# Performance work log

Hardware: AMD Instinct MI355X
Metric: run time of the kernel (lower is better)

The kernel has to match this reference:

```python
import jax, jax.numpy as jnp
import numpy as np

BN_EPS = 1e-5


def knn_idx(x, k):
    # x: (B, N, C) -> (B, N, k) indices of k nearest neighbors (incl. self),
    # DGCNN style: topk of negative squared distance.
    inner = jnp.einsum('bnc,bmc->bnm', x, x)
    sq = jnp.sum(x * x, axis=-1)
    neg_dist = 2.0 * inner - sq[:, :, None] - sq[:, None, :]
    _, idx = jax.lax.top_k(neg_dist, k)
    return idx


def edge_conv(x, W, b, gamma, beta, k):
    # x: (B, N, C); W: (O, 2C). One DGCNN EdgeConv block:
    # knn gather -> concat(nbr - x, x) -> conv1x1 -> BN(batch stats) -> GELU -> max over k.
    idx = knn_idx(x, k)                                   # (B, N, k)
    nbr = jax.vmap(lambda f, i: f[i])(x, idx)             # (B, N, k, C)
    ctr = jnp.broadcast_to(x[:, :, None, :], nbr.shape)
    feat = jnp.concatenate([nbr - ctr, ctr], axis=-1)     # (B, N, k, 2C)
    y = jnp.einsum('bnkc,oc->bnko', feat, W) + b          # conv 1x1
    mean = jnp.mean(y, axis=(0, 1, 2))
    var = jnp.var(y, axis=(0, 1, 2))
    y = (y - mean) * jax.lax.rsqrt(var + BN_EPS) * gamma + beta
    y = jax.nn.gelu(y, approximate=False)                 # torch nn.GELU default (erf)
    return jnp.max(y, axis=2)                             # (B, N, O)


def setup_inputs() -> dict:
    key = jax.random.key(0)
    ks = jax.random.split(key, 8)
    bs, ch, n_patches, n_samples = 4, 6, 32, 256
    dims_in = [12, 32, 64, 128, 256]
    dims_out = [16, 32, 64, 128, 256]
    inp = {'x': jax.random.normal(ks[0], (bs, ch, n_patches, n_samples), dtype=jnp.float32)}
    for i, (ci, co) in enumerate(zip(dims_in, dims_out), start=1):
        wk = jax.random.fold_in(ks[1], i)
        scale = 1.0 / np.sqrt(ci)
        inp[f'W{i}'] = (jax.random.normal(wk, (co, ci), dtype=jnp.float32) * scale)
        inp[f'b{i}'] = jnp.zeros((co,), dtype=jnp.float32)
        inp[f'g{i}'] = jnp.ones((co,), dtype=jnp.float32)
        inp[f'bt{i}'] = jnp.zeros((co,), dtype=jnp.float32)
    inp['k'] = 16
    return inp


def reference(x, W1, b1, g1, bt1, W2, b2, g2, bt2, W3, b3, g3, bt3,
              W4, b4, g4, bt4, W5, b5, g5, bt5, k):
    bs, ch, n_patches, n_samples = x.shape
    # (bs, ch, P, S) -> (bs*P, S, ch)  [channels-last point clouds]
    h = x.transpose(0, 2, 3, 1).reshape(bs * n_patches, n_samples, ch)
    h = edge_conv(h, W1, b1, g1, bt1, k)
    h = edge_conv(h, W2, b2, g2, bt2, k)
    h = edge_conv(h, W3, b3, g3, bt3, k)
    h = edge_conv(h, W4, b4, g4, bt4, k)
    h = edge_conv(h, W5, b5, g5, bt5, k)      # (bs*P, S, dim)
    dim = h.shape[-1]
    h = h.reshape(bs, n_patches, n_samples, dim)
    return h.transpose(0, 3, 1, 2)            # (bs, dim, n_patches, n_samples)
```

## Files before the change

### kernel.cpp

```cpp
#include <hip/hip_runtime.h>
#include <cmath>

#define NPTS 256
#define TOTPTS 32768
#define KNB 16

static const size_t OFF_HA   = 0;
static const size_t OFF_HB   = 4194304;
static const size_t OFF_UZ   = 6291456;
static const size_t OFF_YMAX = 23068672;
static const size_t OFF_YMIN = 31457280;
static const size_t OFF_IDX  = 39845888;
static const size_t OFF_VT   = 40370176;
static const size_t OFF_SUMS = 40458240;

__device__ __forceinline__ float gelu_erf(float v) {
  return 0.5f * v * (1.0f + erff(v * 0.70710678118654752f));
}

__global__ __launch_bounds__(256) void prep_kernel(
    const float* __restrict__ x, float* __restrict__ h0,
    const float* __restrict__ W1, const float* __restrict__ W2, const float* __restrict__ W3,
    const float* __restrict__ W4, const float* __restrict__ W5,
    float* __restrict__ Vt, double* __restrict__ sums) {
  const int stride = gridDim.x * blockDim.x;
  const int tid0 = blockIdx.x * blockDim.x + threadIdx.x;
  for (int id = tid0; id < 196608; id += stride) {
    int ch = id % 6;
    int r  = id / 6;
    int s  = r & 255;
    int p  = (r >> 8) & 31;
    int bs = r >> 13;
    h0[id] = x[(((size_t)(bs * 6 + ch) * 32 + p) << 8) + s];
  }
  for (int id = tid0; id < 87232; id += stride) {
    const float* W; int K, N2, base;
    if (id < 192)        { W = W1; K = 6;   N2 = 32;  base = 0; }
    else if (id < 1216)  { W = W2; K = 16;  N2 = 64;  base = 192; }
    else if (id < 5312)  { W = W3; K = 32;  N2 = 128; base = 1216; }
    else if (id < 21696) { W = W4; K = 64;  N2 = 256; base = 5312; }
    else                 { W = W5; K = 128; N2 = 512; base = 21696; }
    int e = id - base;
    int c = e / N2;
    int j = e - c * N2;
    int O = N2 >> 1;
    Vt[id] = (j < O) ? W[j * 2 * K + c] : W[(j - O) * 2 * K + K + c];
  }
  for (int id = tid0; id < 992; id += stride) sums[id] = 0.0;
}

template<int C>
__global__ __launch_bounds__(256) void sq_kernel(const float* __restrict__ h,
                                                 double* __restrict__ sqd) {
  const int n = blockIdx.x * 256 + threadIdx.x;
  const float* p = h + (size_t)n * C;
  double q0 = 0.0, q1 = 0.0;
  #pragma unroll
  for (int c = 0; c + 1 < C; c += 2) {
    q0 = fma((double)p[c],   (double)p[c],   q0);
    q1 = fma((double)p[c+1], (double)p[c+1], q1);
  }
  #pragma unroll
  for (int c = C & ~1; c < C; ++c) q0 = fma((double)p[c], (double)p[c], q0);
  sqd[n] = q0 + q1;
}

template<int K>
__global__ __launch_bounds__(256) void knn_fused_kernel(const float* __restrict__ h,
                                                        const double* __restrict__ sqd,
                                                        int* __restrict__ idxout) {
  constexpr int KC = (K < 16) ? K : 16;
  __shared__ unsigned long long keys[32 * 257];
  __shared__ __align__(16) float As[KC * 36];
  __shared__ __align__(16) float Bs[KC * 132];
  const int cloud = blockIdx.x >> 3;
  const int i0 = (blockIdx.x & 7) * 32;
  const float* hb = h + (size_t)cloud * NPTS * K;
  const int tid = threadIdx.x;
  const int mm = (tid & 7) * 4;
  const int jj = (tid >> 3) * 4;

  double sqi[4];
  #pragma unroll
  for (int r = 0; r < 4; ++r) sqi[r] = sqd[cloud * NPTS + i0 + mm + r];

  for (int jh = 0; jh < 2; ++jh) {
    const int j0 = jh * 128;
    double acc[4][4] = {{0.0}};
    for (int k0 = 0; k0 < K; k0 += KC) {
      for (int e = tid; e < 32 * KC; e += 256) {
        int am = e / KC, ac = e - am * KC;
        As[ac * 36 + am] = hb[(size_t)(i0 + am) * K + k0 + ac];
      }
      for (int e = tid; e < 128 * KC; e += 256) {
        int bm = e / KC, bc = e - bm * KC;
        Bs[bc * 132 + bm] = hb[(size_t)(j0 + bm) * K + k0 + bc];
      }
      __syncthreads();
      #pragma unroll
      for (int c = 0; c < KC; ++c) {
        float4 av = *(const float4*)(As + c * 36 + mm);
        float4 bv = *(const float4*)(Bs + c * 132 + jj);
        double a0 = (double)av.x, a1 = (double)av.y, a2 = (double)av.z, a3 = (double)av.w;
        double b0 = (double)bv.x, b1 = (double)bv.y, b2 = (double)bv.z, b3 = (double)bv.w;
        acc[0][0] = fma(a0, b0, acc[0][0]);
        acc[0][1] = fma(a0, b1, acc[0][1]);
        acc[0][2] = fma(a0, b2, acc[0][2]);
        acc[0][3] = fma(a0, b3, acc[0][3]);
        acc[1][0] = fma(a1, b0, acc[1][0]);
        acc[1][1] = fma(a1, b1, acc[1][1]);
        acc[1][2] = fma(a1, b2, acc[1][2]);
        acc[1][3] = fma(a1, b3, acc[1][3]);
        acc[2][0] = fma(a2, b0, acc[2][0]);
        acc[2][1] = fma(a2, b1, acc[2][1]);
        acc[2][2] = fma(a2, b2, acc[2][2]);
        acc[2][3] = fma(a2, b3, acc[2][3]);
        acc[3][0] = fma(a3, b0, acc[3][0]);
        acc[3][1] = fma(a3, b1, acc[3][1]);
        acc[3][2] = fma(a3, b2, acc[3][2]);
        acc[3][3] = fma(a3, b3, acc[3][3]);
      }
      __syncthreads();
    }
    double sqj[4];
    #pragma unroll
    for (int s = 0; s < 4; ++s) sqj[s] = sqd[cloud * NPTS + j0 + jj + s];
    #pragma unroll
    for (int r = 0; r < 4; ++r) {
      #pragma unroll
      for (int s = 0; s < 4; ++s) {
        double v = 2.0 * acc[r][s] - sqi[r] - sqj[s];
        int col = j0 + jj + s;
        keys[(mm + r) * 257 + col] =
            (((unsigned long long)__double_as_longlong(v)) & ~0xFFull) |
            (unsigned long long)col;
      }
    }
  }
  __syncthreads();

  const unsigned long long FULL = 0xFFFFFFFFFFFFFFFFull;
  const int wid  = tid >> 6;
  const int lane = tid & 63;
  const int half = lane >> 5;
  const int sub  = lane & 31;
  for (int p = 0; p < 2; ++p) {
    const int rA = p * 16 + wid * 4 + half;
    const int rC = rA + 2;
    const unsigned long long* rp1 = keys + rA * 257 + 8 * sub;
    const unsigned long long* rp2 = keys + rC * 257 + 8 * sub;
    unsigned long long a0 = rp1[0], a1 = rp1[1], a2 = rp1[2], a3 = rp1[3];
    unsigned long long a4 = rp1[4], a5 = rp1[5], a6 = rp1[6], a7 = rp1[7];
    unsigned long long b0 = rp2[0], b1 = rp2[1], b2 = rp2[2], b3 = rp2[3];
    unsigned long long b4 = rp2[4], b5 = rp2[5], b6 = rp2[6], b7 = rp2[7];

    #define CE(X, Y) { unsigned long long lo_ = (X < Y) ? X : Y; \
                       unsigned long long hi_ = (X < Y) ? Y : X; X = lo_; Y = hi_; }
    #define SORT8(v0,v1,v2,v3,v4,v5,v6,v7) \
      CE(v0,v1) CE(v2,v3) CE(v4,v5) CE(v6,v7) \
      CE(v0,v2) CE(v1,v3) CE(v4,v6) CE(v5,v7) \
      CE(v1,v2) CE(v5,v6) \
      CE(v0,v4) CE(v1,v5) CE(v2,v6) CE(v3,v7) \
      CE(v2,v4) CE(v3,v5) \
      CE(v1,v2) CE(v3,v4) CE(v5,v6)
    SORT8(a0,a1,a2,a3,a4,a5,a6,a7)
    SORT8(b0,b1,b2,b3,b4,b5,b6,b7)
    #undef SORT8
    #undef CE

    int keep1 = 0, keep2 = 0;
    for (int round = 0; round < KNB; ++round) {
      unsigned long long m1 = a0, m2 = b0, o;
      o = __shfl_xor(m1, 16); m1 = (o < m1) ? o : m1;
      o = __shfl_xor(m2, 16); m2 = (o < m2) ? o : m2;
      o = __shfl_xor(m1, 8);  m1 = (o < m1) ? o : m1;
      o = __shfl_xor(m2, 8);  m2 = (o < m2) ? o : m2;
      o = __shfl_xor(m1, 4);  m1 = (o < m1) ? o : m1;
      o = __shfl_xor(m2, 4);  m2 = (o < m2) ? o : m2;
      o = __shfl_xor(m1, 2);  m1 = (o < m1) ? o : m1;
      o = __shfl_xor(m2, 2);  m2 = (o < m2) ? o : m2;
      o = __shfl_xor(m1, 1);  m1 = (o < m1) ? o : m1;
      o = __shfl_xor(m2, 1);  m2 = (o < m2) ? o : m2;
      const int col1 = (int)(m1 & 0xFFull);
      const int col2 = (int)(m2 & 0xFFull);
      if ((col1 >> 3) == sub) {
        a0 = a1; a1 = a2; a2 = a3; a3 = a4; a4 = a5; a5 = a6; a6 = a7; a7 = FULL;
      }
      if ((col2 >> 3) == sub) {
        b0 = b1; b1 = b2; b2 = b3; b3 = b4; b4 = b5; b5 = b6; b6 = b7; b7 = FULL;
      }
      if (sub == round) { keep1 = col1; keep2 = col2; }
    }
    if (sub < KNB) {
      const int growA = cloud * NPTS + i0 + rA;
      const int growC = cloud * NPTS + i0 + rC;
      idxout[(size_t)growA * KNB + sub] = cloud * NPTS + keep1;
      idxout[(size_t)growC * KNB + sub] = cloud * NPTS + keep2;
    }
  }
}

template<int K, int N2>
__global__ __launch_bounds__(256) void gemm_uz_kernel(const float* __restrict__ h,
                                                      const float* __restrict__ Vt,
                                                      float* __restrict__ UZ) {
  constexpr int KC = 32;
  constexpr int NBLK = (N2 + 63) / 64;
  __shared__ __align__(16) float As[KC * 68];
  __shared__ __align__(16) float Bs[KC * 68];
  const int m0 = (int)(blockIdx.x / NBLK) * 64;
  const int n0 = (int)(blockIdx.x % NBLK) * 64;
  const int tid = threadIdx.x;
  const int mm = (tid & 15) * 4;
  const int jj = (tid >> 4) * 4;
  float acc[4][4] = {{0.f}};
  for (int k0 = 0; k0 < K; k0 += KC) {
    #pragma unroll
    for (int e = tid; e < 64 * KC; e += 256) {
      int am = e / KC, ac = e - am * KC;
      float v = 0.f;
      if (k0 + ac < K) v = h[(size_t)(m0 + am) * K + k0 + ac];
      As[ac * 68 + am] = v;
    }
    #pragma unroll
    for (int e = tid; e < KC * 64; e += 256) {
      int bj = e & 63, bc = e >> 6;
      float v = 0.f;
      if (k0 + bc < K && n0 + bj < N2) v = Vt[(size_t)(k0 + bc) * N2 + n0 + bj];
      Bs[bc * 68 + bj] = v;
    }
    __syncthreads();
    #pragma unroll
    for (int c = 0; c < KC; ++c) {
      float4 av = *(const float4*)(As + c * 68 + mm);
      float4 bv = *(const float4*)(Bs + c * 68 + jj);
      acc[0][0] = fmaf(av.x, bv.x, acc[0][0]);
      acc[0][1] = fmaf(av.x, bv.y, acc[0][1]);
      acc[0][2] = fmaf(av.x, bv.z, acc[0][2]);
      acc[0][3] = fmaf(av.x, bv.w, acc[0][3]);
      acc[1][0] = fmaf(av.y, bv.x, acc[1][0]);
      acc[1][1] = fmaf(av.y, bv.y, acc[1][1]);
      acc[1][2] = fmaf(av.y, bv.z, acc[1][2]);
      acc[1][3] = fmaf(av.y, bv.w, acc[1][3]);
      acc[2][0] = fmaf(av.z, bv.x, acc[2][0]);
      acc[2][1] = fmaf(av.z, bv.y, acc[2][1]);
      acc[2][2] = fmaf(av.z, bv.z, acc[2][2]);
      acc[2][3] = fmaf(av.z, bv.w, acc[2][3]);
      acc[3][0] = fmaf(av.w, bv.x, acc[3][0]);
      acc[3][1] = fmaf(av.w, bv.y, acc[3][1]);
      acc[3][2] = fmaf(av.w, bv.z, acc[3][2]);
      acc[3][3] = fmaf(av.w, bv.w, acc[3][3]);
    }
    __syncthreads();
  }
  if (n0 + jj < N2) {
    #pragma unroll
    for (int i = 0; i < 4; ++i) {
      float4 v = make_float4(acc[i][0], acc[i][1], acc[i][2], acc[i][3]);
      *(float4*)(UZ + (size_t)(m0 + mm + i) * N2 + n0 + jj) = v;
    }
  }
}

template<int K, int N2>
__global__ __launch_bounds__(256) void gemm_big_kernel(const float* __restrict__ h,
                                                       const float* __restrict__ Vt,
                                                       float* __restrict__ UZ) {
  constexpr int KC = 32;
  constexpr int PAD = 132;
  constexpr int NBLK = N2 / 128;
  __shared__ __align__(16) float As[KC * PAD];
  __shared__ __align__(16) float Bs[KC * PAD];
  const int m0 = (int)(blockIdx.x / NBLK) * 128;
  const int n0 = (int)(blockIdx.x % NBLK) * 128;
  const int tid = threadIdx.x;
  const int ra = (tid & 15) * 4;
  const int ca = (tid >> 4) * 4;
  float acc[8][8];
  #pragma unroll
  for (int i = 0; i < 8; ++i)
    #pragma unroll
    for (int j = 0; j < 8; ++j) acc[i][j] = 0.f;

  for (int k0 = 0; k0 < K; k0 += KC) {
    #pragma unroll
    for (int q = 0; q < 4; ++q) {
      int idx = tid + 256 * q;
      int am = idx >> 3;
      int aq = idx & 7;
      float4 v = *(const float4*)(h + (size_t)(m0 + am) * K + k0 + 4 * aq);
      As[(4 * aq + 0) * PAD + am] = v.x;
      As[(4 * aq + 1) * PAD + am] = v.y;
      As[(4 * aq + 2) * PAD + am] = v.z;
      As[(4 * aq + 3) * PAD + am] = v.w;
    }
    #pragma unroll
    for (int q = 0; q < 4; ++q) {
      int idx = tid + 256 * q;
      int bk = idx >> 5;
      int bq = idx & 31;
      *(float4*)(Bs + bk * PAD + 4 * bq) =
          *(const float4*)(Vt + (size_t)(k0 + bk) * N2 + n0 + 4 * bq);
    }
    __syncthreads();
    #pragma unroll
    for (int cc = 0; cc < KC; ++cc) {
      float4 a0 = *(const float4*)(As + cc * PAD + ra);
      float4 a1 = *(const float4*)(As + cc * PAD + 64 + ra);
      float4 b0 = *(const float4*)(Bs + cc * PAD + ca);
      float4 b1 = *(const float4*)(Bs + cc * PAD + 64 + ca);
      float av[8] = {a0.x, a0.y, a0.z, a0.w, a1.x, a1.y, a1.z, a1.w};
      float bv[8] = {b0.x, b0.y, b0.z, b0.w, b1.x, b1.y, b1.z, b1.w};
      #pragma unroll
      for (int i = 0; i < 8; ++i)
        #pragma unroll
        for (int j = 0; j < 8; ++j)
          acc[i][j] = fmaf(av[i], bv[j], acc[i][j]);
    }
    __syncthreads();
  }
  #pragma unroll
  for (int i = 0; i < 8; ++i) {
    int row = m0 + ((i < 4) ? (ra + i) : (64 + ra + (i - 4)));
    float4 v0 = make_float4(acc[i][0], acc[i][1], acc[i][2], acc[i][3]);
    float4 v1 = make_float4(acc[i][4], acc[i][5], acc[i][6], acc[i][7]);
    *(float4*)(UZ + (size_t)row * N2 + n0 + ca) = v0;
    *(float4*)(UZ + (size_t)row * N2 + n0 + 64 + ca) = v1;
  }
}

template<int O, int GRID>
__global__ __launch_bounds__(256) void combine_kernel(const float* __restrict__ UZ,
    const int* __restrict__ idx, const float* __restrict__ bias,
    float* __restrict__ ymax, float* __restrict__ ymin, double* __restrict__ partials) {
  constexpr int TPP = O / 4;
  constexpr int PPI = 256 / TPP;
  constexpr int PPB = TOTPTS / GRID;
  constexpr int ITERS = PPB / PPI;
  static_assert(ITERS >= 1, "grid too large for this O");
  constexpr int BPC = GRID / 128;
  __shared__ double red[256];
  const int tid = threadIdx.x;
  const int oc  = tid % TPP;
  const int sub = tid / TPP;
  const int x    = blockIdx.x & 7;
  const int slot = blockIdx.x >> 3;
  const int c    = x + 8 * (slot / BPC);
  const int w    = slot % BPC;
  const int base = c * NPTS + w * PPB;
  const float4* UZ4 = (const float4*)UZ;
  float4* ymx4 = (float4*)ymax;
  float4* ymn4 = (float4*)ymin;
  const float4 b4 = ((const float4*)bias)[oc];
  double a1x = 0.0, a1y = 0.0, a1z = 0.0, a1w = 0.0;
  double a2x = 0.0, a2y = 0.0, a2z = 0.0, a2w = 0.0;
  for (int it = 0; it < ITERS; ++it) {
    int n = base + it * PPI + sub;
    const int* ip = idx + (size_t)n * KNB;
    float4 un = UZ4[(size_t)n * (O / 2) + oc];
    float4 zn = UZ4[(size_t)n * (O / 2) + O / 4 + oc];
    float4 w4 = make_float4(zn.x - un.x + b4.x, zn.y - un.y + b4.y,
                            zn.z - un.z + b4.z, zn.w - un.w + b4.w);
    float4 mx = make_float4(-INFINITY, -INFINITY, -INFINITY, -INFINITY);
    float4 mn = make_float4(INFINITY, INFINITY, INFINITY, INFINITY);
    float4 s1 = make_float4(0.f, 0.f, 0.f, 0.f);
    float4 s2 = make_float4(0.f, 0.f, 0.f, 0.f);
    #pragma unroll
    for (int kk = 0; kk < KNB; ++kk) {
      int j = ip[kk];
      float4 uv = UZ4[(size_t)j * (O / 2) + oc];
      mx.x = fmaxf(mx.x, uv.x); mx.y = fmaxf(mx.y, uv.y);
      mx.z = fmaxf(mx.z, uv.z); mx.w = fmaxf(mx.w, uv.w);
      mn.x = fminf(mn.x, uv.x); mn.y = fminf(mn.y, uv.y);
      mn.z = fminf(mn.z, uv.z); mn.w = fminf(mn.w, uv.w);
      s1.x += uv.x; s1.y += uv.y; s1.z += uv.z; s1.w += uv.w;
      s2.x = fmaf(uv.x, uv.x, s2.x); s2.y = fmaf(uv.y, uv.y, s2.y);
      s2.z = fmaf(uv.z, uv.z, s2.z); s2.w = fmaf(uv.w, uv.w, s2.w);
    }
    ymx4[(size_t)n * (O / 4) + oc] = make_float4(mx.x + w4.x, mx.y + w4.y, mx.z + w4.z, mx.w + w4.w);
    ymn4[(size_t)n * (O / 4) + oc] = make_float4(mn.x + w4.x, mn.y + w4.y, mn.z + w4.z, mn.w + w4.w);
    a1x += (double)(s1.x + 16.f * w4.x);
    a1y += (double)(s1.y + 16.f * w4.y);
    a1z += (double)(s1.z + 16.f * w4.z);
    a1w += (double)(s1.w + 16.f * w4.w);
    a2x += (double)(s2.x + 2.f * w4.x * s1.x + 16.f * (w4.x * w4.x));
    a2y += (double)(s2.y + 2.f * w4.y * s1.y + 16.f * (w4.y * w4.y));
    a2z += (double)(s2.z + 2.f * w4.z * s1.z + 16.f * (w4.z * w4.z));
    a2w += (double)(s2.w + 2.f * w4.w * s1.w + 16.f * (w4.w * w4.w));
  }
  #define REDUCE_ONE(VAL, CH_OFF)                                        \
    red[tid] = (VAL);                                                    \
    __syncthreads();                                                     \
    if (tid < TPP) {                                                     \
      double t = 0.0;                                                    \
      _Pragma("unroll")                                                  \
      for (int q = 0; q < PPI; ++q) t += red[q * TPP + tid];             \
      partials[(size_t)((CH_OFF) + 4 * tid) * GRID + blockIdx.x] = t;    \
    }                                                                    \
    __syncthreads();
  REDUCE_ONE(a1x, 0)
  REDUCE_ONE(a1y, 1)
  REDUCE_ONE(a1z, 2)
  REDUCE_ONE(a1w, 3)
  REDUCE_ONE(a2x, O + 0)
  REDUCE_ONE(a2y, O + 1)
  REDUCE_ONE(a2z, O + 2)
  REDUCE_ONE(a2w, O + 3)
  #undef REDUCE_ONE
}

template<int NB>
__global__ __launch_bounds__(256) void reduce_sums_kernel(const double* __restrict__ part,
                                                          double* __restrict__ sums) {
  __shared__ double red[256];
  const int ch = blockIdx.x;
  const double* p = part + (size_t)ch * NB;
  double t = 0.0;
  for (int i = threadIdx.x; i < NB; i += 256) t += p[i];
  red[threadIdx.x] = t;
  __syncthreads();
  #pragma unroll
  for (int s = 128; s > 0; s >>= 1) {
    if (threadIdx.x < s) red[threadIdx.x] += red[threadIdx.x + s];
    __syncthreads();
  }
  if (threadIdx.x == 0) sums[ch] = red[0];
}

template<int O>
__global__ __launch_bounds__(256) void apply_kernel(const float* __restrict__ ymax,
    const float* __restrict__ ymin, const double* __restrict__ sums,
    const float* __restrict__ g, const float* __restrict__ bt, float* __restrict__ hout) {
  const int tid = blockIdx.x * 256 + threadIdx.x;
  const int o = tid & (O - 1);
  double m = sums[o] * (1.0 / 524288.0);
  double v = fma(-m, m, sums[O + o] * (1.0 / 524288.0));
  float A = g[o] / sqrtf((float)v + 1e-5f);
  float Cc = fmaf(-(float)m, A, bt[o]);
  float r1 = gelu_erf(fmaf(A, ymax[tid], Cc));
  float r2 = gelu_erf(fmaf(A, ymin[tid], Cc));
  hout[tid] = fmaxf(r1, r2);
}

__global__ __launch_bounds__(256) void apply_final_kernel(const float* __restrict__ ymax,
    const float* __restrict__ ymin, const double* __restrict__ sums,
    const float* __restrict__ g, const float* __restrict__ bt, float* __restrict__ out) {
  constexpr int O = 256;
  __shared__ float tile[64 * 65];
  const int bo = blockIdx.x & 3;
  const int bn = blockIdx.x >> 2;
  const int n0 = bn * 64, o0 = bo * 64;
  const int lane = threadIdx.x & 63;
  const int grp = threadIdx.x >> 6;
  {
    const int oc = o0 + lane;
    double m = sums[oc] * (1.0 / 524288.0);
    double v = fma(-m, m, sums[O + oc] * (1.0 / 524288.0));
    float A = g[oc] / sqrtf((float)v + 1e-5f);
    float Cc = fmaf(-(float)m, A, bt[oc]);
    #pragma unroll
    for (int q = 0; q < 16; ++q) {
      int r = grp * 16 + q;
      size_t src = (size_t)(n0 + r) * O + oc;
      float r1 = gelu_erf(fmaf(A, ymax[src], Cc));
      float r2 = gelu_erf(fmaf(A, ymin[src], Cc));
      tile[r * 65 + lane] = fmaxf(r1, r2);
    }
  }
  __syncthreads();
  const int s0 = n0 & 255;
  const int p  = (n0 >> 8) & 31;
  const int bs = n0 >> 13;
  size_t basei = ((size_t)(bs * 256 + o0) * 32 + p) * 256 + s0;
  #pragma unroll
  for (int q = 0; q < 16; ++q) {
    int c = grp * 16 + q;
    out[basei + (size_t)c * 8192 + lane] = tile[lane * 65 + c];
  }
}

extern "C" void kernel_launch(void* const* d_in, const int* in_sizes, int n_in,
                              void* d_out, int out_size, void* d_ws, size_t ws_size,
                              hipStream_t stream) {
  (void)in_sizes; (void)n_in; (void)out_size; (void)ws_size;
  const float* x   = (const float*)d_in[0];
  const float* W1  = (const float*)d_in[1];
  const float* b1  = (const float*)d_in[2];
  const float* g1  = (const float*)d_in[3];
  const float* bt1 = (const float*)d_in[4];
  const float* W2  = (const float*)d_in[5];
  const float* b2  = (const float*)d_in[6];
  const float* g2  = (const float*)d_in[7];
  const float* bt2 = (const float*)d_in[8];
  const float* W3  = (const float*)d_in[9];
  const float* b3  = (const float*)d_in[10];
  const float* g3  = (const float*)d_in[11];
  const float* bt3 = (const float*)d_in[12];
  const float* W4  = (const float*)d_in[13];
  const float* b4  = (const float*)d_in[14];
  const float* g4  = (const float*)d_in[15];
  const float* bt4 = (const float*)d_in[16];
  const float* W5  = (const float*)d_in[17];
  const float* b5  = (const float*)d_in[18];
  const float* g5  = (const float*)d_in[19];
  const float* bt5 = (const float*)d_in[20];

  float* ws    = (float*)d_ws;
  float* hA    = ws + OFF_HA;
  float* hB    = ws + OFF_HB;
  float* UZ    = ws + OFF_UZ;
  float* ymx   = ws + OFF_YMAX;
  float* ymn   = ws + OFF_YMIN;
  int*   idxb  = (int*)(ws + OFF_IDX);
  float* Vt    = ws + OFF_VT;
  double* sums = (double*)(ws + OFF_SUMS);
  double* sqd  = (double*)ymx;
  double* partA = (double*)hA;
  double* partB = (double*)hB;

  prep_kernel<<<256, 256, 0, stream>>>(x, hA, W1, W2, W3, W4, W5, Vt, sums);

  sq_kernel<6><<<128, 256, 0, stream>>>(hA, sqd);
  knn_fused_kernel<6><<<1024, 256, 0, stream>>>(hA, sqd, idxb);
  gemm_uz_kernel<6, 32><<<512, 256, 0, stream>>>(hA, Vt + 0, UZ);
  combine_kernel<16, 512><<<512, 256, 0, stream>>>(UZ, idxb, b1, ymx, ymn, partA);
  reduce_sums_kernel<512><<<32, 256, 0, stream>>>(partA, sums + 0);
  apply_kernel<16><<<2048, 256, 0, stream>>>(ymx, ymn, sums + 0, g1, bt1, hB);

  sq_kernel<16><<<128, 256, 0, stream>>>(hB, sqd);
  knn_fused_kernel<16><<<1024, 256, 0, stream>>>(hB, sqd, idxb);
  gemm_uz_kernel<16, 64><<<512, 256, 0, stream>>>(hB, Vt + 192, UZ);
  combine_kernel<32, 1024><<<1024, 256, 0, stream>>>(UZ, idxb, b2, ymx, ymn, partB);
  reduce_sums_kernel<1024><<<64, 256, 0, stream>>>(partB, sums + 32);
  apply_kernel<32><<<4096, 256, 0, stream>>>(ymx, ymn, sums + 32, g2, bt2, hA);

  sq_kernel<32><<<128, 256, 0, stream>>>(hA, sqd);
  knn_fused_kernel<32><<<1024, 256, 0, stream>>>(hA, sqd, idxb);
  gemm_big_kernel<32, 128><<<256, 256, 0, stream>>>(hA, Vt + 1216, UZ);
  combine_kernel<64, 2048><<<2048, 256, 0, stream>>>(UZ, idxb, b3, ymx, ymn, partA);
  reduce_sums_kernel<2048><<<128, 256, 0, stream>>>(partA, sums + 96);
  apply_kernel<64><<<8192, 256, 0, stream>>>(ymx, ymn, sums + 96, g3, bt3, hB);

  sq_kernel<64><<<128, 256, 0, stream>>>(hB, sqd);
  knn_fused_kernel<64><<<1024, 256, 0, stream>>>(hB, sqd, idxb);
  gemm_big_kernel<64, 256><<<512, 256, 0, stream>>>(hB, Vt + 5312, UZ);
  combine_kernel<128, 2048><<<2048, 256, 0, stream>>>(UZ, idxb, b4, ymx, ymn, partB);
  reduce_sums_kernel<2048><<<256, 256, 0, stream>>>(partB, sums + 224);
  apply_kernel<128><<<16384, 256, 0, stream>>>(ymx, ymn, sums + 224, g4, bt4, hA);

  sq_kernel<128><<<128, 256, 0, stream>>>(hA, sqd);
  knn_fused_kernel<128><<<1024, 256, 0, stream>>>(hA, sqd, idxb);
  gemm_big_kernel<128, 512><<<1024, 256, 0, stream>>>(hA, Vt + 21696, UZ);
  combine_kernel<256, 2048><<<2048, 256, 0, stream>>>(UZ, idxb, b5, ymx, ymn, partA);
  reduce_sums_kernel<2048><<<512, 256, 0, stream>>>(partA, sums + 480);
  apply_final_kernel<<<2048, 256, 0, stream>>>(ymx, ymn, sums + 480, g5, bt5, (float*)d_out);
}
```

Baseline: 784.7 us.

## Restructure knn kernel to keep distance keys in registers with 16-row strips

The fused kNN kernel now handles 16 query rows per block against all 256 candidates. Each thread computes a 2x8 tile of fp64 dot products whose layout matches the per-lane ownership the warp top-k selection needs, so the keys no longer pass through a 32x257 64-bit shared-memory buffer and the extra barrier. Block indices are remapped so blocks of the same cloud land on the same XCD, which should improve L2 reuse, and the grid doubles to 2048 blocks. The trade-off is that each block reloads all 256 candidate points for only 16 query rows, which adds redundant global and LDS loading work.

```diff
diff --git a/kernel.cpp b/kernel.cpp
--- a/kernel.cpp
+++ b/kernel.cpp
@@ -69,134 +69,134 @@
 __global__ __launch_bounds__(256) void knn_fused_kernel(const float* __restrict__ h,
                                                         const double* __restrict__ sqd,
                                                         int* __restrict__ idxout) {
-  constexpr int KC = (K < 16) ? K : 16;
-  __shared__ unsigned long long keys[32 * 257];
-  __shared__ __align__(16) float As[KC * 36];
-  __shared__ __align__(16) float Bs[KC * 132];
-  const int cloud = blockIdx.x >> 3;
-  const int i0 = (blockIdx.x & 7) * 32;
+  constexpr int KC  = (K < 32) ? K : 32;
+  constexpr int AST = 18;
+  constexpr int BST = 260;
+  __shared__ __align__(16) float As[KC * AST];
+  __shared__ __align__(16) float Bs[KC * BST];
+  const int xcd   = blockIdx.x & 7;
+  const int q     = blockIdx.x >> 3;
+  const int cloud = xcd + 8 * (q >> 4);
+  const int strip = q & 15;
+  const int i0    = strip * 16;
   const float* hb = h + (size_t)cloud * NPTS * K;
   const int tid = threadIdx.x;
-  const int mm = (tid & 7) * 4;
-  const int jj = (tid >> 3) * 4;
-
-  double sqi[4];
-  #pragma unroll
-  for (int r = 0; r < 4; ++r) sqi[r] = sqd[cloud * NPTS + i0 + mm + r];
-
-  for (int jh = 0; jh < 2; ++jh) {
-    const int j0 = jh * 128;
-    double acc[4][4] = {{0.0}};
-    for (int k0 = 0; k0 < K; k0 += KC) {
-      for (int e = tid; e < 32 * KC; e += 256) {
-        int am = e / KC, ac = e - am * KC;
-        As[ac * 36 + am] = hb[(size_t)(i0 + am) * K + k0 + ac];
-      }
-      for (int e = tid; e < 128 * KC; e += 256) {
-        int bm = e / KC, bc = e - bm * KC;
-        Bs[bc * 132 + bm] = hb[(size_t)(j0 + bm) * K + k0 + bc];
-      }
-      __syncthreads();
-      #pragma unroll
-      for (int c = 0; c < KC; ++c) {
-        float4 av = *(const float4*)(As + c * 36 + mm);
-        float4 bv = *(const float4*)(Bs + c * 132 + jj);
-        double a0 = (double)av.x, a1 = (double)av.y, a2 = (double)av.z, a3 = (double)av.w;
-        double b0 = (double)bv.x, b1 = (double)bv.y, b2 = (double)bv.z, b3 = (double)bv.w;
-        acc[0][0] = fma(a0, b0, acc[0][0]);
-        acc[0][1] = fma(a0, b1, acc[0][1]);
-        acc[0][2] = fma(a0, b2, acc[0][2]);
-        acc[0][3] = fma(a0, b3, acc[0][3]);
-        acc[1][0] = fma(a1, b0, acc[1][0]);
-        acc[1][1] = fma(a1, b1, acc[1][1]);
-        acc[1][2] = fma(a1, b2, acc[1][2]);
-        acc[1][3] = fma(a1, b3, acc[1][3]);
-        acc[2][0] = fma(a2, b0, acc[2][0]);
-        acc[2][1] = fma(a2, b1, acc[2][1]);
-        acc[2][2] = fma(a2, b2, acc[2][2]);
-        acc[2][3] = fma(a2, b3, acc[2][3]);
-        acc[3][0] = fma(a3, b0, acc[3][0]);
-        acc[3][1] = fma(a3, b1, acc[3][1]);
-        acc[3][2] = fma(a3, b2, acc[3][2]);
-        acc[3][3] = fma(a3, b3, acc[3][3]);
-      }
-      __syncthreads();
-    }
-    double sqj[4];
-    #pragma unroll
-    for (int s = 0; s < 4; ++s) sqj[s] = sqd[cloud * NPTS + j0 + jj + s];
-    #pragma unroll
-    for (int r = 0; r < 4; ++r) {
-      #pragma unroll
-      for (int s = 0; s < 4; ++s) {
-        double v = 2.0 * acc[r][s] - sqi[r] - sqj[s];
-        int col = j0 + jj + s;
-        keys[(mm + r) * 257 + col] =
-            (((unsigned long long)__double_as_longlong(v)) & ~0xFFull) |
-            (unsigned long long)col;
-      }
-    }
-  }
-  __syncthreads();
+  const int c   = tid & 31;
+  const int g   = tid >> 5;
+
+  double acc[2][8];
+  #pragma unroll
+  for (int r = 0; r < 2; ++r)
+    #pragma unroll
+    for (int j = 0; j < 8; ++j) acc[r][j] = 0.0;
+
+  for (int k0 = 0; k0 < K; k0 += KC) {
+    for (int e = tid; e < 16 * KC; e += 256) {
+      int am = e / KC, ac = e - am * KC;
+      As[ac * AST + am] = hb[(size_t)(i0 + am) * K + k0 + ac];
+    }
+    for (int e = tid; e < 256 * KC; e += 256) {
+      int bm = e / KC, bc = e - bm * KC;
+      Bs[bc * BST + bm] = hb[(size_t)bm * K + k0 + bc];
+    }
+    __syncthreads();
+    #pragma unroll
+    for (int kk = 0; kk < KC; ++kk) {
+      float2 af  = *(const float2*)(As + kk * AST + 2 * g);
+      float4 bf0 = *(const float4*)(Bs + kk * BST + 8 * c);
+      float4 bf1 = *(const float4*)(Bs + kk * BST + 8 * c + 4);
+      double a0 = (double)af.x, a1 = (double)af.y;
+      double b0 = (double)bf0.x, b1 = (double)bf0.y, b2 = (double)bf0.z, b3 = (double)bf0.w;
+      double b4 = (double)bf1.x, b5 = (double)bf1.y, b6 = (double)bf1.z, b7 = (double)bf1.w;
+      acc[0][0] = fma(a0, b0, acc[0][0]);
+      acc[0][1] = fma(a0, b1, acc[0][1]);
+      acc[0][2] = fma(a0, b2, acc[0][2]);
+      acc[0][3] = fma(a0, b3, acc[0][3]);
+      acc[0][4] = fma(a0, b4, acc[0][4]);
+      acc[0][5] = fma(a0, b5, acc[0][5]);
+      acc[0][6] = fma(a0, b6, acc[0][6]);
+      acc[0][7] = fma(a0, b7, acc[0][7]);
+      acc[1][0] = fma(a1, b0, acc[1][0]);
+      acc[1][1] = fma(a1, b1, acc[1][1]);
+      acc[1][2] = fma(a1, b2, acc[1][2]);
+      acc[1][3] = fma(a1, b3, acc[1][3]);
+      acc[1][4] = fma(a1, b4, acc[1][4]);
+      acc[1][5] = fma(a1, b5, acc[1][5]);
+      acc[1][6] = fma(a1, b6, acc[1][6]);
+      acc[1][7] = fma(a1, b7, acc[1][7]);
+    }
+    __syncthreads();
+  }
+
+  const double sqi0 = sqd[cloud * NPTS + i0 + 2 * g];
+  const double sqi1 = sqd[cloud * NPTS + i0 + 2 * g + 1];
+  double sqj[8];
+  #pragma unroll
+  for (int j = 0; j < 8; ++j) sqj[j] = sqd[cloud * NPTS + 8 * c + j];
+  const unsigned cb = 8u * (unsigned)c;
+
+  #define MK(P, Q) ((((unsigned long long)__double_as_longlong(P)) & ~0xFFull) | (cb + (Q)))
+  unsigned long long a0 = MK(2.0 * acc[0][0] - sqi0 - sqj[0], 0u);
+  unsigned long long a1 = MK(2.0 * acc[0][1] - sqi0 - sqj[1], 1u);
+  unsigned long long a2 = MK(2.0 * acc[0][2] - sqi0 - sqj[2], 2u);
+  unsigned long long a3 = MK(2.0 * acc[0][3] - sqi0 - sqj[3], 3u);
+  unsigned long long a4 = MK(2.0 * acc[0][4] - sqi0 - sqj[4], 4u);
+  unsigned long long a5 = MK(2.0 * acc[0][5] - sqi0 - sqj[5], 5u);
+  unsigned long long a6 = MK(2.0 * acc[0][6] - sqi0 - sqj[6], 6u);
+  unsigned long long a7 = MK(2.0 * acc[0][7] - sqi0 - sqj[7], 7u);
+  unsigned long long b0 = MK(2.0 * acc[1][0] - sqi1 - sqj[0], 0u);
+  unsigned long long b1 = MK(2.0 * acc[1][1] - sqi1 - sqj[1], 1u);
+  unsigned long long b2 = MK(2.0 * acc[1][2] - sqi1 - sqj[2], 2u);
+  unsigned long long b3 = MK(2.0 * acc[1][3] - sqi1 - sqj[3], 3u);
+  unsigned long long b4 = MK(2.0 * acc[1][4] - sqi1 - sqj[4], 4u);
+  unsigned long long b5 = MK(2.0 * acc[1][5] - sqi1 - sqj[5], 5u);
+  unsigned long long b6 = MK(2.0 * acc[1][6] - sqi1 - sqj[6], 6u);
+  unsigned long long b7 = MK(2.0 * acc[1][7] - sqi1 - sqj[7], 7u);
+  #undef MK
+
+  #define CE(X, Y) { unsigned long long lo_ = (X < Y) ? X : Y; \
+                     unsigned long long hi_ = (X < Y) ? Y : X; X = lo_; Y = hi_; }
+  #define SORT8(v0,v1,v2,v3,v4,v5,v6,v7) \
+    CE(v0,v1) CE(v2,v3) CE(v4,v5) CE(v6,v7) \
+    CE(v0,v2) CE(v1,v3) CE(v4,v6) CE(v5,v7) \
+    CE(v1,v2) CE(v5,v6) \
+    CE(v0,v4) CE(v1,v5) CE(v2,v6) CE(v3,v7) \
+    CE(v2,v4) CE(v3,v5) \
+    CE(v1,v2) CE(v3,v4) CE(v5,v6)
+  SORT8(a0,a1,a2,a3,a4,a5,a6,a7)
+  SORT8(b0,b1,b2,b3,b4,b5,b6,b7)
+  #undef SORT8
+  #undef CE
 
   const unsigned long long FULL = 0xFFFFFFFFFFFFFFFFull;
-  const int wid  = tid >> 6;
-  const int lane = tid & 63;
-  const int half = lane >> 5;
-  const int sub  = lane & 31;
-  for (int p = 0; p < 2; ++p) {
-    const int rA = p * 16 + wid * 4 + half;
-    const int rC = rA + 2;
-    const unsigned long long* rp1 = keys + rA * 257 + 8 * sub;
-    const unsigned long long* rp2 = keys + rC * 257 + 8 * sub;
-    unsigned long long a0 = rp1[0], a1 = rp1[1], a2 = rp1[2], a3 = rp1[3];
-    unsigned long long a4 = rp1[4], a5 = rp1[5], a6 = rp1[6], a7 = rp1[7];
-    unsigned long long b0 = rp2[0], b1 = rp2[1], b2 = rp2[2], b3 = rp2[3];
-    unsigned long long b4 = rp2[4], b5 = rp2[5], b6 = rp2[6], b7 = rp2[7];
-
-    #define CE(X, Y) { unsigned long long lo_ = (X < Y) ? X : Y; \
-                       unsigned long long hi_ = (X < Y) ? Y : X; X = lo_; Y = hi_; }
-    #define SORT8(v0,v1,v2,v3,v4,v5,v6,v7) \
-      CE(v0,v1) CE(v2,v3) CE(v4,v5) CE(v6,v7) \
-      CE(v0,v2) CE(v1,v3) CE(v4,v6) CE(v5,v7) \
-      CE(v1,v2) CE(v5,v6) \
-      CE(v0,v4) CE(v1,v5) CE(v2,v6) CE(v3,v7) \
-      CE(v2,v4) CE(v3,v5) \
-      CE(v1,v2) CE(v3,v4) CE(v5,v6)
-    SORT8(a0,a1,a2,a3,a4,a5,a6,a7)
-    SORT8(b0,b1,b2,b3,b4,b5,b6,b7)
-    #undef SORT8
-    #undef CE
-
-    int keep1 = 0, keep2 = 0;
-    for (int round = 0; round < KNB; ++round) {
-      unsigned long long m1 = a0, m2 = b0, o;
-      o = __shfl_xor(m1, 16); m1 = (o < m1) ? o : m1;
-      o = __shfl_xor(m2, 16); m2 = (o < m2) ? o : m2;
-      o = __shfl_xor(m1, 8);  m1 = (o < m1) ? o : m1;
-      o = __shfl_xor(m2, 8);  m2 = (o < m2) ? o : m2;
-      o = __shfl_xor(m1, 4);  m1 = (o < m1) ? o : m1;
-      o = __shfl_xor(m2, 4);  m2 = (o < m2) ? o : m2;
-      o = __shfl_xor(m1, 2);  m1 = (o < m1) ? o : m1;
-      o = __shfl_xor(m2, 2);  m2 = (o < m2) ? o : m2;
-      o = __shfl_xor(m1, 1);  m1 = (o < m1) ? o : m1;
-      o = __shfl_xor(m2, 1);  m2 = (o < m2) ? o : m2;
-      const int col1 = (int)(m1 & 0xFFull);
-      const int col2 = (int)(m2 & 0xFFull);
-      if ((col1 >> 3) == sub) {
-        a0 = a1; a1 = a2; a2 = a3; a3 = a4; a4 = a5; a5 = a6; a6 = a7; a7 = FULL;
-      }
-      if ((col2 >> 3) == sub) {
-        b0 = b1; b1 = b2; b2 = b3; b3 = b4; b4 = b5; b5 = b6; b6 = b7; b7 = FULL;
-      }
-      if (sub == round) { keep1 = col1; keep2 = col2; }
-    }
-    if (sub < KNB) {
-      const int growA = cloud * NPTS + i0 + rA;
-      const int growC = cloud * NPTS + i0 + rC;
-      idxout[(size_t)growA * KNB + sub] = cloud * NPTS + keep1;
-      idxout[(size_t)growC * KNB + sub] = cloud * NPTS + keep2;
-    }
+  const int sub = c;
+  int keep1 = 0, keep2 = 0;
+  for (int round = 0; round < KNB; ++round) {
+    unsigned long long m1 = a0, m2 = b0, o;
+    o = __shfl_xor(m1, 16); m1 = (o < m1) ? o : m1;
+    o = __shfl_xor(m2, 16); m2 = (o < m2) ? o : m2;
+    o = __shfl_xor(m1, 8);  m1 = (o < m1) ? o : m1;
+    o = __shfl_xor(m2, 8);  m2 = (o < m2) ? o : m2;
+    o = __shfl_xor(m1, 4);  m1 = (o < m1) ? o : m1;
+    o = __shfl_xor(m2, 4);  m2 = (o < m2) ? o : m2;
+    o = __shfl_xor(m1, 2);  m1 = (o < m1) ? o : m1;
+    o = __shfl_xor(m2, 2);  m2 = (o < m2) ? o : m2;
+    o = __shfl_xor(m1, 1);  m1 = (o < m1) ? o : m1;
+    o = __shfl_xor(m2, 1);  m2 = (o < m2) ? o : m2;
+    const int col1 = (int)(m1 & 0xFFull);
+    const int col2 = (int)(m2 & 0xFFull);
+    if ((col1 >> 3) == sub) {
+      a0 = a1; a1 = a2; a2 = a3; a3 = a4; a4 = a5; a5 = a6; a6 = a7; a7 = FULL;
+    }
+    if ((col2 >> 3) == sub) {
+      b0 = b1; b1 = b2; b2 = b3; b3 = b4; b4 = b5; b5 = b6; b6 = b7; b7 = FULL;
+    }
+    if (sub == round) { keep1 = col1; keep2 = col2; }
+  }
+  if (sub < KNB) {
+    const int rowA = cloud * NPTS + i0 + 2 * g;
+    idxout[(size_t)rowA * KNB + sub]       = cloud * NPTS + keep1;
+    idxout[(size_t)(rowA + 1) * KNB + sub] = cloud * NPTS + keep2;
   }
 }
 
@@ -521,35 +521,35 @@
   prep_kernel<<<256, 256, 0, stream>>>(x, hA, W1, W2, W3, W4, W5, Vt, sums);
 
   sq_kernel<6><<<128, 256, 0, stream>>>(hA, sqd);
-  knn_fused_kernel<6><<<1024, 256, 0, stream>>>(hA, sqd, idxb);
+  knn_fused_kernel<6><<<2048, 256, 0, stream>>>(hA, sqd, idxb);
   gemm_uz_kernel<6, 32><<<512, 256, 0, stream>>>(hA, Vt + 0, UZ);
   combine_kernel<16, 512><<<512, 256, 0, stream>>>(UZ, idxb, b1, ymx, ymn, partA);
   reduce_sums_kernel<512><<<32, 256, 0, stream>>>(partA, sums + 0);
   apply_kernel<16><<<2048, 256, 0, stream>>>(ymx, ymn, sums + 0, g1, bt1, hB);
 
   sq_kernel<16><<<128, 256, 0, stream>>>(hB, sqd);
-  knn_fused_kernel<16><<<1024, 256, 0, stream>>>(hB, sqd, idxb);
+  knn_fused_kernel<16><<<2048, 256, 0, stream>>>(hB, sqd, idxb);
   gemm_uz_kernel<16, 64><<<512, 256, 0, stream>>>(hB, Vt + 192, UZ);
   combine_kernel<32, 1024><<<1024, 256, 0, stream>>>(UZ, idxb, b2, ymx, ymn, partB);
   reduce_sums_kernel<1024><<<64, 256, 0, stream>>>(partB, sums + 32);
   apply_kernel<32><<<4096, 256, 0, stream>>>(ymx, ymn, sums + 32, g2, bt2, hA);
 
   sq_kernel<32><<<128, 256, 0, stream>>>(hA, sqd);
-  knn_fused_kernel<32><<<1024, 256, 0, stream>>>(hA, sqd, idxb);
+  knn_fused_kernel<32><<<2048, 256, 0, stream>>>(hA, sqd, idxb);
   gemm_big_kernel<32, 128><<<256, 256, 0, stream>>>(hA, Vt + 1216, UZ);
   combine_kernel<64, 2048><<<2048, 256, 0, stream>>>(UZ, idxb, b3, ymx, ymn, partA);
   reduce_sums_kernel<2048><<<128, 256, 0, stream>>>(partA, sums + 96);
   apply_kernel<64><<<8192, 256, 0, stream>>>(ymx, ymn, sums + 96, g3, bt3, hB);
 
   sq_kernel<64><<<128, 256, 0, stream>>>(hB, sqd);
-  knn_fused_kernel<64><<<1024, 256, 0, stream>>>(hB, sqd, idxb);
+  knn_fused_kernel<64><<<2048, 256, 0, stream>>>(hB, sqd, idxb);
   gemm_big_kernel<64, 256><<<512, 256, 0, stream>>>(hB, Vt + 5312, UZ);
   combine_kernel<128, 2048><<<2048, 256, 0, stream>>>(UZ, idxb, b4, ymx, ymn, partB);
   reduce_sums_kernel<2048><<<256, 256, 0, stream>>>(partB, sums + 224);
   apply_kernel<128><<<16384, 256, 0, stream>>>(ymx, ymn, sums + 224, g4, bt4, hA);
 
   sq_kernel<128><<<128, 256, 0, stream>>>(hA, sqd);
-  knn_fused_kernel<128><<<1024, 256, 0, stream>>>(hA, sqd, idxb);
+  knn_fused_kernel<128><<<2048, 256, 0, stream>>>(hA, sqd, idxb);
   gemm_big_kernel<128, 512><<<1024, 256, 0, stream>>>(hA, Vt + 21696, UZ);
   combine_kernel<256, 2048><<<2048, 256, 0, stream>>>(UZ, idxb, b5, ymx, ymn, partA);
   reduce_sums_kernel<2048><<<512, 256, 0, stream>>>(partA, sums + 480);
```

Result: faster. 666.3 us (-15.1%).
